# Optimization experiments

Hardware: AMD Instinct MI355X
Metric: run time of the kernel (lower is better)

The kernel has to match this reference:

```python
import jax, jax.numpy as jnp
import numpy as np

B, DIM1, DIM2, LATENT, T = 16, 1024, 1024, 512, 2048  # T == video_feat_dim
LN_EPS = 1e-5


def setup_inputs() -> dict:
    key = jax.random.key(0)
    ks = jax.random.split(key, 8)
    def xavier(k, shape):
        fan_out, fan_in = shape
        std = float(np.sqrt(2.0 / (fan_in + fan_out)))
        return jax.random.normal(k, shape, dtype=jnp.float32) * std
    return {
        "input1": jax.random.normal(ks[0], (B, DIM1, T), dtype=jnp.float32),
        "input2": jax.random.normal(ks[1], (B, DIM2, T), dtype=jnp.float32),
        "theta_w": xavier(ks[2], (LATENT, DIM2)),
        "theta_b": jnp.zeros((LATENT,), jnp.float32),
        "phi_w": xavier(ks[3], (LATENT, DIM1)),
        "phi_b": jnp.zeros((LATENT,), jnp.float32),
        "g_w": xavier(ks[4], (LATENT, DIM1)),
        "g_b": jnp.zeros((LATENT,), jnp.float32),
        "ln_gamma": jnp.ones((LATENT, T), jnp.float32),
        "ln_beta": jnp.zeros((LATENT, T), jnp.float32),
        "out_w": xavier(ks[5], (DIM2, LATENT)),
        "out_b": jnp.zeros((DIM2,), jnp.float32),
    }


def reference(input1, input2, theta_w, theta_b, phi_w, phi_b, g_w, g_b,
              ln_gamma, ln_beta, out_w, out_b):
    # 1x1 Conv1d == channel-wise matmul
    theta_x = jnp.einsum('ld,bdt->btl', theta_w, input2) + theta_b          # [B,T2,L]
    phi_x = jnp.einsum('ld,bdt->blt', phi_w, input1) + phi_b[:, None]       # [B,L,T1]
    scores = jnp.einsum('btl,bls->bts', theta_x, phi_x)                      # [B,T2,T1] (unscaled)
    p = jax.nn.softmax(scores, axis=-1)
    g_x = jnp.einsum('ld,bdt->btl', g_w, input1) + g_b                       # [B,T1,L]
    t_x = jnp.einsum('bts,bsl->blt', p, g_x)                                 # [B,L,T2]
    # LayerNorm over the last two dims jointly [LATENT, T]
    mu = jnp.mean(t_x, axis=(1, 2), keepdims=True)
    var = jnp.var(t_x, axis=(1, 2), keepdims=True)
    h = (t_x - mu) * jax.lax.rsqrt(var + LN_EPS) * ln_gamma + ln_beta
    h = jax.nn.relu(h)
    w_t = jnp.einsum('ol,blt->bot', out_w, h) + out_b[None, :, None]         # [B,DIM2,T2]
    return w_t + input2
```

## Files before the change

### kernel.cpp

```cpp
#include <hip/hip_runtime.h>
#include <hip/hip_bf16.h>

#define BB 16
#define D1 1024
#define D2 1024
#define LL 512
#define TT 2048
#define LN_EPS 1e-5f

typedef unsigned short u16;
typedef __attribute__((ext_vector_type(8))) _Float16 half8;
typedef __attribute__((ext_vector_type(4))) float f32x4;
typedef __attribute__((ext_vector_type(4))) unsigned int u32x4;

__device__ __forceinline__ u16 f2h(float v) {
    _Float16 h = (_Float16)v;
    return *(u16*)&h;
}
__device__ __forceinline__ float h2f(u16 u) {
    return (float)(*(const _Float16*)&u);
}

__device__ __forceinline__ void gload_lds16(const void* g, void* l) {
    __builtin_amdgcn_global_load_lds((const __attribute__((address_space(1))) void*)g,
                                     (__attribute__((address_space(3))) void*)l, 16, 0, 0);
}

#define MEMFENCE asm volatile("" ::: "memory")
__device__ __forceinline__ void block_barrier() {
    MEMFENCE; __builtin_amdgcn_s_barrier(); MEMFENCE;
}

template<int BIAS, int OMODE>
__global__ __launch_bounds__(512, 1) void nt_gemm(
    const u16* __restrict__ A, const u16* __restrict__ B,
    long sAb, long sBb, long sCb,
    int N, int Kd, int gx, int gy,
    const float* __restrict__ bias,
    void* __restrict__ out0,
    const float* __restrict__ resid, long sRb)
{
    __shared__ __align__(16) u16 smem[65536];

    const int nwg = gridDim.x;
    const int id = blockIdx.x;
    const int swz = (id & 7) * (nwg >> 3) + (id >> 3);
    const int bx = swz % gx;
    const int byz = swz / gx;
    const int by = byz % gy;
    const int b = byz / gy;

    const int tid = threadIdx.x;
    const long arow0 = (long)by * 256;
    const long brow0 = (long)bx * 256;
    const u16* Ab = A + (long)b * sAb + arow0 * Kd;
    const u16* Bb = B + (long)b * sBb + brow0 * Kd;

    const int wave = tid >> 6, lane = tid & 63;
    const int mh = wave >> 2;
    const int wm = mh * 128;
    const int wn = (wave & 3) * 64;
    const int lm = lane & 15, kg = lane >> 4;

    const int ntile = Kd >> 6;

    auto STAGE = [&](int buf, long k0) {
        u16* Ad = smem + buf * 32768;
        u16* Bd = Ad + 16384;
#pragma unroll
        for (int sw = 0; sw < 4; ++sw) {
            int idx = sw * 512 + tid;
            int m = idx >> 3, s = idx & 7;
            int gs = s ^ (m & 7);
            gload_lds16(Ab + k0 + (long)m * Kd + gs * 8, Ad + idx * 8);
        }
#pragma unroll
        for (int sw = 0; sw < 4; ++sw) {
            int idx = sw * 512 + tid;
            int m = idx >> 3, s = idx & 7;
            int gs = s ^ (m & 7);
            gload_lds16(Bb + k0 + (long)m * Kd + gs * 8, Bd + idx * 8);
        }
    };

    f32x4 acc[8][4];
#pragma unroll
    for (int i = 0; i < 8; ++i)
#pragma unroll
        for (int j = 0; j < 4; ++j) acc[i][j] = (f32x4){0.f, 0.f, 0.f, 0.f};

    STAGE(0, 0);
    if (ntile > 1) STAGE(1, 64);

    half8 a_[4][2], b_[2][2];

#define LOADA(ms_) do { \
    _Pragma("unroll") for (int f = 0; f < 4; ++f) \
    _Pragma("unroll") for (int kf = 0; kf < 2; ++kf) { \
        int mr = wm + (ms_) * 64 + f * 16 + lm; \
        int ss = (kf * 4 + kg) ^ (mr & 7); \
        a_[f][kf] = *(const half8*)(Ac + mr * 64 + ss * 8); } } while (0)
#define LOADB(ns_) do { \
    _Pragma("unroll") for (int f = 0; f < 2; ++f) \
    _Pragma("unroll") for (int kf = 0; kf < 2; ++kf) { \
        int nr = wn + (ns_) * 32 + f * 16 + lm; \
        int ss = (kf * 4 + kg) ^ (nr & 7); \
        b_[f][kf] = *(const half8*)(Bc + nr * 64 + ss * 8); } } while (0)
#define PH_MFMA(ms_, ns_) do { \
    block_barrier(); \
    asm volatile("s_waitcnt lgkmcnt(0)" ::: "memory"); \
    __builtin_amdgcn_sched_barrier(0); \
    __builtin_amdgcn_s_setprio(1); \
    _Pragma("unroll") for (int i = 0; i < 4; ++i) \
    _Pragma("unroll") for (int j = 0; j < 2; ++j) \
    _Pragma("unroll") for (int kf = 0; kf < 2; ++kf) \
        acc[(ms_) * 4 + i][(ns_) * 2 + j] = __builtin_amdgcn_mfma_f32_16x16x32_f16( \
            a_[i][kf], b_[j][kf], acc[(ms_) * 4 + i][(ns_) * 2 + j], 0, 0, 0); \
    __builtin_amdgcn_s_setprio(0); \
    block_barrier(); \
} while (0)

    for (int t = 0; t < ntile; ++t) {
        const int c = t & 1;
        const u16* Ac = smem + c * 32768;
        const u16* Bc = Ac + 16384;
        if (t + 1 < ntile) { asm volatile("s_waitcnt vmcnt(8)" ::: "memory"); }
        else               { asm volatile("s_waitcnt vmcnt(0)" ::: "memory"); }
        block_barrier();

        LOADA(0); LOADB(0); PH_MFMA(0, 0);
        LOADA(1);           PH_MFMA(1, 0);
        LOADB(1);           PH_MFMA(1, 1);
        LOADA(0);           PH_MFMA(0, 1);

        if (t + 2 < ntile) STAGE(c, (long)(t + 2) * 64);
    }
#undef LOADA
#undef LOADB
#undef PH_MFMA

    float* Cs = (float*)smem;
#pragma unroll
    for (int p = 0; p < 2; ++p) {
        __syncthreads();
        if (mh == p) {
#pragma unroll
            for (int ms = 0; ms < 2; ++ms)
#pragma unroll
                for (int i = 0; i < 4; ++i)
#pragma unroll
                    for (int ns = 0; ns < 2; ++ns)
#pragma unroll
                        for (int j = 0; j < 2; ++j)
#pragma unroll
                            for (int r = 0; r < 4; ++r) {
                                int row = ms * 64 + i * 16 + kg * 4 + r;
                                int col = wn + ns * 32 + j * 16 + lm;
                                Cs[row * 256 + (col ^ ((row & 7) << 2))] = acc[ms * 4 + i][ns * 2 + j][r];
                            }
        }
        __syncthreads();
        if (OMODE == 0 || OMODE == 3) {
#pragma unroll
            for (int it = 0; it < 16; ++it) {
                int elem = it * 512 + tid;
                int row = elem >> 6, c4 = elem & 63;
                int grow = (int)arow0 + p * 128 + row;
                int gcol = (int)brow0 + c4 * 4;
                f32x4 v = *(const f32x4*)&Cs[row * 256 + ((c4 ^ (row & 7)) << 2)];
                if (BIAS == 1) v += bias[grow];
                if (BIAS == 2) v += *(const f32x4*)(bias + gcol);
                long off = (long)b * sCb + (long)grow * N + gcol;
                if (OMODE == 3) {
                    f32x4 rv = __builtin_nontemporal_load(
                        (const f32x4*)(resid + (long)b * sRb + (long)grow * N + gcol));
                    v += rv;
                    __builtin_nontemporal_store(v, (f32x4*)((float*)out0 + off));
                } else {
                    *(f32x4*)((float*)out0 + off) = v;
                }
            }
        } else {
#pragma unroll
            for (int it = 0; it < 8; ++it) {
                int elem = it * 512 + tid;
                int row = elem >> 5, c8 = elem & 31;
                int grow = (int)arow0 + p * 128 + row;
                int gcol = (int)brow0 + c8 * 8;
                int g0 = (c8 * 2) ^ (row & 7);
                int g1 = (c8 * 2 + 1) ^ (row & 7);
                f32x4 u0 = *(const f32x4*)&Cs[row * 256 + g0 * 4];
                f32x4 u1 = *(const f32x4*)&Cs[row * 256 + g1 * 4];
                float vv[8] = {u0.x, u0.y, u0.z, u0.w, u1.x, u1.y, u1.z, u1.w};
                if (BIAS == 1) {
                    float bb = bias[grow];
#pragma unroll
                    for (int q = 0; q < 8; ++q) vv[q] += bb;
                }
                if (BIAS == 2) {
#pragma unroll
                    for (int q = 0; q < 8; ++q) vv[q] += bias[gcol + q];
                }
                union { u16 u[8]; u32x4 v4; } pk;
#pragma unroll
                for (int q = 0; q < 8; ++q) pk.u[q] = f2h(vv[q]);
                long off = (long)b * sCb + (long)grow * N + gcol;
                *(u32x4*)((u16*)out0 + off) = pk.v4;
            }
        }
    }
}

__global__ __launch_bounds__(256) void transpose_h(const float* __restrict__ in,
                                                   u16* __restrict__ o16, int D, int T) {
    __shared__ float tile[64][65];
    int b = blockIdx.z;
    const float* src = in + (long)b * D * T;
    long obase = (long)b * D * T;
    int t0 = blockIdx.x * 64, d0 = blockIdx.y * 64;
    int tx = threadIdx.x & 63, ty = threadIdx.x >> 6;
#pragma unroll
    for (int i = 0; i < 64; i += 4)
        tile[ty + i][tx] = __builtin_nontemporal_load(&src[(long)(d0 + ty + i) * T + t0 + tx]);
    __syncthreads();
#pragma unroll
    for (int i = 0; i < 64; i += 4) {
        long o = obase + (long)(t0 + ty + i) * D + d0 + tx;
        o16[o] = f2h(tile[tx][ty + i]);
    }
}

__global__ __launch_bounds__(256) void transpose_f32(const float* __restrict__ in,
                                                     float* __restrict__ out, int R, int C) {
    __shared__ float tile[64][65];
    int c0 = blockIdx.x * 64, r0 = blockIdx.y * 64;
    int tx = threadIdx.x & 63, ty = threadIdx.x >> 6;
#pragma unroll
    for (int i = 0; i < 64; i += 4)
        tile[ty + i][tx] = in[(long)(r0 + ty + i) * C + c0 + tx];
    __syncthreads();
#pragma unroll
    for (int i = 0; i < 64; i += 4)
        out[(long)(c0 + ty + i) * R + r0 + tx] = tile[tx][ty + i];
}

__global__ __launch_bounds__(256) void conv_w(const float* __restrict__ w,
                                              u16* __restrict__ h, int n) {
    int i = blockIdx.x * 256 + threadIdx.x;
    if (i < n) h[i] = f2h(w[i]);
}

__global__ __launch_bounds__(256) void softmax_rows(const float* __restrict__ S, u16* __restrict__ P) {
    long row = (long)blockIdx.z * TT + blockIdx.x;
    const float* s = S + row * TT;
    u16* p = P + row * TT;
    int tid = threadIdx.x;
    f32x4 v0 = *(const f32x4*)(s + tid * 8);
    f32x4 v1 = *(const f32x4*)(s + tid * 8 + 4);
    float x[8] = {v0.x, v0.y, v0.z, v0.w, v1.x, v1.y, v1.z, v1.w};
    float m = x[0];
#pragma unroll
    for (int j = 1; j < 8; ++j) m = fmaxf(m, x[j]);
#pragma unroll
    for (int off = 32; off; off >>= 1) m = fmaxf(m, __shfl_xor(m, off, 64));
    __shared__ float red[8];
    int wave = tid >> 6, lane = tid & 63;
    if (lane == 0) red[wave] = m;
    __syncthreads();
    m = fmaxf(fmaxf(red[0], red[1]), fmaxf(red[2], red[3]));
    float e[8]; float sum = 0.f;
#pragma unroll
    for (int j = 0; j < 8; ++j) { e[j] = __expf(x[j] - m); sum += e[j]; }
#pragma unroll
    for (int off = 32; off; off >>= 1) sum += __shfl_xor(sum, off, 64);
    if (lane == 0) red[4 + wave] = sum;
    __syncthreads();
    sum = red[4] + red[5] + red[6] + red[7];
    float inv = 1.f / sum;
    union { u16 u[8]; u32x4 v4; } pk;
#pragma unroll
    for (int j = 0; j < 8; ++j) pk.u[j] = f2h(e[j] * inv);
    *(u32x4*)(p + tid * 8) = pk.v4;
}

__global__ void zero32(float* p) { p[threadIdx.x] = 0.f; }

__global__ __launch_bounds__(256) void ln_partial(const u16* __restrict__ TXp, float* __restrict__ sums) {
    int b = blockIdx.z;
    const u16* x = TXp + (long)b * (LL * TT) + (long)blockIdx.x * 32768;
    int tid = threadIdx.x;
    float s = 0.f, sq = 0.f;
#pragma unroll 4
    for (int j = 0; j < 16; ++j) {
        u32x4 v = *(const u32x4*)(x + (j * 256 + tid) * 8);
        unsigned w[4] = {v.x, v.y, v.z, v.w};
#pragma unroll
        for (int q = 0; q < 4; ++q) {
            float a = h2f((u16)(w[q] & 0xffff));
            float c = h2f((u16)(w[q] >> 16));
            s += a + c;
            sq += a * a + c * c;
        }
    }
#pragma unroll
    for (int off = 32; off; off >>= 1) { s += __shfl_xor(s, off, 64); sq += __shfl_xor(sq, off, 64); }
    __shared__ float rs[8];
    int wave = tid >> 6, lane = tid & 63;
    if (lane == 0) { rs[wave] = s; rs[4 + wave] = sq; }
    __syncthreads();
    if (tid == 0) {
        atomicAdd(&sums[b * 2], rs[0] + rs[1] + rs[2] + rs[3]);
        atomicAdd(&sums[b * 2 + 1], rs[4] + rs[5] + rs[6] + rs[7]);
    }
}

__global__ __launch_bounds__(256) void ln_apply(const u16* __restrict__ TXp, const float* __restrict__ sums,
                                                const float* __restrict__ gT, const float* __restrict__ bT,
                                                u16* __restrict__ H) {
    int b = blockIdx.z;
    const float n = (float)(LL * TT);
    float mu = sums[b * 2] / n;
    float var = sums[b * 2 + 1] / n - mu * mu;
    float rstd = rsqrtf(var + LN_EPS);
    long base = (long)b * (LL * TT);
    long idx = ((long)blockIdx.x * 256 + threadIdx.x) * 8;
    u32x4 xv = *(const u32x4*)(TXp + base + idx);
    unsigned w[4] = {xv.x, xv.y, xv.z, xv.w};
    f32x4 g0 = *(const f32x4*)(gT + idx);
    f32x4 g1 = *(const f32x4*)(gT + idx + 4);
    f32x4 b0 = *(const f32x4*)(bT + idx);
    f32x4 b1 = *(const f32x4*)(bT + idx + 4);
    float g[8] = {g0.x, g0.y, g0.z, g0.w, g1.x, g1.y, g1.z, g1.w};
    float be[8] = {b0.x, b0.y, b0.z, b0.w, b1.x, b1.y, b1.z, b1.w};
    union { u16 u[8]; u32x4 v; } pk;
#pragma unroll
    for (int q = 0; q < 4; ++q) {
        float a = h2f((u16)(w[q] & 0xffff));
        float c = h2f((u16)(w[q] >> 16));
        float oa = fmaxf((a - mu) * rstd * g[q * 2] + be[q * 2], 0.f);
        float oc = fmaxf((c - mu) * rstd * g[q * 2 + 1] + be[q * 2 + 1], 0.f);
        pk.u[q * 2] = f2h(oa);
        pk.u[q * 2 + 1] = f2h(oc);
    }
    *(u32x4*)(H + base + idx) = pk.v;
}

extern "C" void kernel_launch(void* const* d_in, const int* in_sizes, int n_in,
                              void* d_out, int out_size, void* d_ws, size_t ws_size,
                              hipStream_t stream) {
    const float* input1  = (const float*)d_in[0];
    const float* input2  = (const float*)d_in[1];
    const float* theta_w = (const float*)d_in[2];
    const float* theta_b = (const float*)d_in[3];
    const float* phi_w   = (const float*)d_in[4];
    const float* phi_b   = (const float*)d_in[5];
    const float* g_w     = (const float*)d_in[6];
    const float* g_b     = (const float*)d_in[7];
    const float* ln_gamma= (const float*)d_in[8];
    const float* ln_beta = (const float*)d_in[9];
    const float* out_w   = (const float*)d_in[10];
    const float* out_b   = (const float*)d_in[11];
    float* out = (float*)d_out;

    char* ws = (char*)d_ws;
    const size_t MB = 1ull << 20;
    u16*  Xt     = (u16*)(ws + 0);
    float* scores= (float*)(ws + 0);
    u16*  pmat   = (u16*)(ws + 64 * MB);
    u16*  Qf     = (u16*)(ws + 192 * MB);
    u16*  Kf     = (u16*)(ws + 224 * MB);
    u16*  Vt     = (u16*)(ws + 256 * MB);
    u16*  TX     = (u16*)(ws + 288 * MB);
    u16*  H      = (u16*)(ws + 320 * MB);
    u16*  thw    = (u16*)(ws + 352 * MB);
    u16*  phw    = (u16*)(ws + 353 * MB);
    u16*  gww    = (u16*)(ws + 354 * MB);
    u16*  oww    = (u16*)(ws + 355 * MB);
    float* gammaT= (float*)(ws + 356 * MB);
    float* betaT = (float*)(ws + 360 * MB);
    float* sums  = (float*)(ws + 364 * MB);

    dim3 blk(256), blk5(512);

    conv_w<<<dim3((LL * D2 + 255) / 256), blk, 0, stream>>>(theta_w, thw, LL * D2);
    conv_w<<<dim3((LL * D1 + 255) / 256), blk, 0, stream>>>(phi_w, phw, LL * D1);
    conv_w<<<dim3((LL * D1 + 255) / 256), blk, 0, stream>>>(g_w, gww, LL * D1);
    conv_w<<<dim3((D2 * LL + 255) / 256), blk, 0, stream>>>(out_w, oww, D2 * LL);
    transpose_f32<<<dim3(TT / 64, LL / 64, 1), blk, 0, stream>>>(ln_gamma, gammaT, LL, TT);
    transpose_f32<<<dim3(TT / 64, LL / 64, 1), blk, 0, stream>>>(ln_beta, betaT, LL, TT);

    transpose_h<<<dim3(TT / 64, D2 / 64, BB), blk, 0, stream>>>(input2, Xt, D2, TT);
    nt_gemm<2, 1><<<dim3((LL / 256) * (TT / 256) * BB), blk5, 0, stream>>>(
        Xt, thw, (long)TT * D2, 0, (long)TT * LL, LL, D2, LL / 256, TT / 256,
        theta_b, Qf, nullptr, 0);

    transpose_h<<<dim3(TT / 64, D1 / 64, BB), blk, 0, stream>>>(input1, Xt, D1, TT);
    nt_gemm<2, 1><<<dim3((LL / 256) * (TT / 256) * BB), blk5, 0, stream>>>(
        Xt, phw, (long)TT * D1, 0, (long)TT * LL, LL, D1, LL / 256, TT / 256,
        phi_b, Kf, nullptr, 0);
    nt_gemm<1, 1><<<dim3((TT / 256) * (LL / 256) * BB), blk5, 0, stream>>>(
        gww, Xt, 0, (long)TT * D1, (long)LL * TT, TT, D1, TT / 256, LL / 256,
        g_b, Vt, nullptr, 0);

    for (int c = 0; c < 4; ++c) {
        long qoff = (long)c * 4 * TT * LL;
        nt_gemm<0, 0><<<dim3((TT / 256) * (TT / 256) * 4), blk5, 0, stream>>>(
            Qf + qoff, Kf + qoff, (long)TT * LL, (long)TT * LL, (long)TT * TT,
            TT, LL, TT / 256, TT / 256, nullptr, scores, nullptr, 0);
        softmax_rows<<<dim3(TT, 1, 4), blk, 0, stream>>>(scores, pmat + (long)c * 4 * TT * TT);
    }
    nt_gemm<0, 1><<<dim3((LL / 256) * (TT / 256) * BB), blk5, 0, stream>>>(
        pmat, Vt, (long)TT * TT, (long)LL * TT, (long)TT * LL,
        LL, TT, LL / 256, TT / 256, nullptr, TX, nullptr, 0);

    zero32<<<dim3(1), dim3(32), 0, stream>>>(sums);
    ln_partial<<<dim3(32, 1, BB), blk, 0, stream>>>(TX, sums);
    ln_apply<<<dim3(512, 1, BB), blk, 0, stream>>>(TX, sums, gammaT, betaT, H);

    nt_gemm<1, 3><<<dim3((TT / 256) * (D2 / 256) * BB), blk5, 0, stream>>>(
        oww, H, 0, (long)TT * LL, (long)D2 * TT, TT, LL, TT / 256, D2 / 256,
        out_b, out, input2, (long)D2 * TT);
}
```

Measured before the change: 603.3 us.

## Add 128x128 GEMM variant and interleave P·V per chunk to shrink probability buffer

```diff
diff --git a/kernel.cpp b/kernel.cpp
--- a/kernel.cpp
+++ b/kernel.cpp
@@ -211,6 +211,146 @@
     }
 }
 
+__device__ __forceinline__ void stage_tile_sm(const u16* __restrict__ g, int ldk, u16* lds, int tid) {
+#pragma unroll
+    for (int it = 0; it < 4; ++it) {
+        int idx = it * 256 + tid;
+        int m = idx >> 3, s = idx & 7;
+        int gs = s ^ (m & 7);
+        gload_lds16(g + (long)m * ldk + gs * 8, lds + idx * 8);
+    }
+}
+
+template<int BIAS, int OMODE>
+__global__ __launch_bounds__(256, 4) void nt_gemm_sm(
+    const u16* __restrict__ A, const u16* __restrict__ B,
+    long sAb, long sBb, long sCb,
+    int N, int Kd, int gx, int gy,
+    const float* __restrict__ bias,
+    void* __restrict__ out0,
+    const float* __restrict__ resid, long sRb)
+{
+    __shared__ __align__(16) u16 smem[2 * 128 * 64];
+    u16* As = smem;
+    u16* Bs = smem + 128 * 64;
+
+    const int nwg = gridDim.x;
+    const int id = blockIdx.x;
+    const int swz = (id & 7) * (nwg >> 3) + (id >> 3);
+    const int bx = swz % gx;
+    const int byz = swz / gx;
+    const int by = byz % gy;
+    const int b = byz / gy;
+
+    const int tid = threadIdx.x;
+    const long arow0 = (long)by * 128;
+    const long brow0 = (long)bx * 128;
+    const u16* Ab = A + (long)b * sAb + arow0 * Kd;
+    const u16* Bb = B + (long)b * sBb + brow0 * Kd;
+
+    const int wave = tid >> 6, lane = tid & 63;
+    const int wm = (wave >> 1) * 64, wn = (wave & 1) * 64;
+    const int lm = lane & 15, kg = lane >> 4;
+
+    f32x4 acc[4][4];
+#pragma unroll
+    for (int i = 0; i < 4; ++i)
+#pragma unroll
+        for (int j = 0; j < 4; ++j) acc[i][j] = (f32x4){0.f, 0.f, 0.f, 0.f};
+
+    for (int k0 = 0; k0 < Kd; k0 += 64) {
+        stage_tile_sm(Ab + k0, Kd, As, tid);
+        stage_tile_sm(Bb + k0, Kd, Bs, tid);
+        __syncthreads();
+#pragma unroll
+        for (int ks = 0; ks < 2; ++ks) {
+            half8 af[4], bf[4];
+#pragma unroll
+            for (int f = 0; f < 4; ++f) {
+                int mr = wm + f * 16 + lm;
+                int as_ = (ks * 4 + kg) ^ (mr & 7);
+                af[f] = *(const half8*)(As + mr * 64 + as_ * 8);
+                int nr = wn + f * 16 + lm;
+                int bs_ = (ks * 4 + kg) ^ (nr & 7);
+                bf[f] = *(const half8*)(Bs + nr * 64 + bs_ * 8);
+            }
+#pragma unroll
+            for (int i = 0; i < 4; ++i)
+#pragma unroll
+                for (int j = 0; j < 4; ++j)
+                    acc[i][j] = __builtin_amdgcn_mfma_f32_16x16x32_f16(af[i], bf[j], acc[i][j], 0, 0, 0);
+        }
+        __syncthreads();
+    }
+
+    float* Cs = (float*)smem;
+#pragma unroll
+    for (int p = 0; p < 2; ++p) {
+        if (p) __syncthreads();
+        if (wm == p * 64) {
+#pragma unroll
+            for (int i = 0; i < 4; ++i)
+#pragma unroll
+                for (int j = 0; j < 4; ++j)
+#pragma unroll
+                    for (int r = 0; r < 4; ++r) {
+                        int row = i * 16 + kg * 4 + r;
+                        int col = wn + j * 16 + lm;
+                        Cs[row * 128 + (col ^ ((row & 7) << 2))] = acc[i][j][r];
+                    }
+        }
+        __syncthreads();
+        if (OMODE == 0 || OMODE == 3) {
+#pragma unroll
+            for (int rr = 0; rr < 8; ++rr) {
+                int elem = rr * 256 + tid;
+                int row = elem >> 5, c4 = elem & 31;
+                int grow = (int)arow0 + p * 64 + row;
+                int gcol = (int)brow0 + c4 * 4;
+                f32x4 v = *(const f32x4*)&Cs[row * 128 + ((c4 ^ (row & 7)) << 2)];
+                if (BIAS == 1) v += bias[grow];
+                if (BIAS == 2) v += *(const f32x4*)(bias + gcol);
+                long off = (long)b * sCb + (long)grow * N + gcol;
+                if (OMODE == 3) {
+                    f32x4 rv = __builtin_nontemporal_load(
+                        (const f32x4*)(resid + (long)b * sRb + (long)grow * N + gcol));
+                    v += rv;
+                    __builtin_nontemporal_store(v, (f32x4*)((float*)out0 + off));
+                } else {
+                    *(f32x4*)((float*)out0 + off) = v;
+                }
+            }
+        } else {
+#pragma unroll
+            for (int rr = 0; rr < 4; ++rr) {
+                int elem = rr * 256 + tid;
+                int row = elem >> 4, c8 = elem & 15;
+                int grow = (int)arow0 + p * 64 + row;
+                int gcol = (int)brow0 + c8 * 8;
+                int g0 = (c8 * 2) ^ (row & 7);
+                int g1 = (c8 * 2 + 1) ^ (row & 7);
+                f32x4 u0 = *(const f32x4*)&Cs[row * 128 + g0 * 4];
+                f32x4 u1 = *(const f32x4*)&Cs[row * 128 + g1 * 4];
+                float vv[8] = {u0.x, u0.y, u0.z, u0.w, u1.x, u1.y, u1.z, u1.w};
+                if (BIAS == 1) {
+                    float bb = bias[grow];
+#pragma unroll
+                    for (int q = 0; q < 8; ++q) vv[q] += bb;
+                }
+                if (BIAS == 2) {
+#pragma unroll
+                    for (int q = 0; q < 8; ++q) vv[q] += bias[gcol + q];
+                }
+                union { u16 u[8]; u32x4 v4; } pk;
+#pragma unroll
+                for (int q = 0; q < 8; ++q) pk.u[q] = f2h(vv[q]);
+                long off = (long)b * sCb + (long)grow * N + gcol;
+                *(u32x4*)((u16*)out0 + off) = pk.v4;
+            }
+        }
+    }
+}
+
 __global__ __launch_bounds__(256) void transpose_h(const float* __restrict__ in,
                                                    u16* __restrict__ o16, int D, int T) {
     __shared__ float tile[64][65];
@@ -367,18 +507,18 @@
     u16*  Xt     = (u16*)(ws + 0);
     float* scores= (float*)(ws + 0);
     u16*  pmat   = (u16*)(ws + 64 * MB);
-    u16*  Qf     = (u16*)(ws + 192 * MB);
-    u16*  Kf     = (u16*)(ws + 224 * MB);
-    u16*  Vt     = (u16*)(ws + 256 * MB);
-    u16*  TX     = (u16*)(ws + 288 * MB);
-    u16*  H      = (u16*)(ws + 320 * MB);
-    u16*  thw    = (u16*)(ws + 352 * MB);
-    u16*  phw    = (u16*)(ws + 353 * MB);
-    u16*  gww    = (u16*)(ws + 354 * MB);
-    u16*  oww    = (u16*)(ws + 355 * MB);
-    float* gammaT= (float*)(ws + 356 * MB);
-    float* betaT = (float*)(ws + 360 * MB);
-    float* sums  = (float*)(ws + 364 * MB);
+    u16*  Qf     = (u16*)(ws + 96 * MB);
+    u16*  Kf     = (u16*)(ws + 128 * MB);
+    u16*  Vt     = (u16*)(ws + 160 * MB);
+    u16*  TX     = (u16*)(ws + 192 * MB);
+    u16*  H      = (u16*)(ws + 224 * MB);
+    u16*  thw    = (u16*)(ws + 256 * MB);
+    u16*  phw    = (u16*)(ws + 257 * MB);
+    u16*  gww    = (u16*)(ws + 258 * MB);
+    u16*  oww    = (u16*)(ws + 259 * MB);
+    float* gammaT= (float*)(ws + 260 * MB);
+    float* betaT = (float*)(ws + 264 * MB);
+    float* sums  = (float*)(ws + 268 * MB);
 
     dim3 blk(256), blk5(512);
 
@@ -390,16 +530,16 @@
     transpose_f32<<<dim3(TT / 64, LL / 64, 1), blk, 0, stream>>>(ln_beta, betaT, LL, TT);
 
     transpose_h<<<dim3(TT / 64, D2 / 64, BB), blk, 0, stream>>>(input2, Xt, D2, TT);
-    nt_gemm<2, 1><<<dim3((LL / 256) * (TT / 256) * BB), blk5, 0, stream>>>(
-        Xt, thw, (long)TT * D2, 0, (long)TT * LL, LL, D2, LL / 256, TT / 256,
+    nt_gemm_sm<2, 1><<<dim3((LL / 128) * (TT / 128) * BB), blk, 0, stream>>>(
+        Xt, thw, (long)TT * D2, 0, (long)TT * LL, LL, D2, LL / 128, TT / 128,
         theta_b, Qf, nullptr, 0);
 
     transpose_h<<<dim3(TT / 64, D1 / 64, BB), blk, 0, stream>>>(input1, Xt, D1, TT);
-    nt_gemm<2, 1><<<dim3((LL / 256) * (TT / 256) * BB), blk5, 0, stream>>>(
-        Xt, phw, (long)TT * D1, 0, (long)TT * LL, LL, D1, LL / 256, TT / 256,
+    nt_gemm_sm<2, 1><<<dim3((LL / 128) * (TT / 128) * BB), blk, 0, stream>>>(
+        Xt, phw, (long)TT * D1, 0, (long)TT * LL, LL, D1, LL / 128, TT / 128,
         phi_b, Kf, nullptr, 0);
-    nt_gemm<1, 1><<<dim3((TT / 256) * (LL / 256) * BB), blk5, 0, stream>>>(
-        gww, Xt, 0, (long)TT * D1, (long)LL * TT, TT, D1, TT / 256, LL / 256,
+    nt_gemm_sm<1, 1><<<dim3((TT / 128) * (LL / 128) * BB), blk, 0, stream>>>(
+        gww, Xt, 0, (long)TT * D1, (long)LL * TT, TT, D1, TT / 128, LL / 128,
         g_b, Vt, nullptr, 0);
 
     for (int c = 0; c < 4; ++c) {
@@ -407,17 +547,17 @@
         nt_gemm<0, 0><<<dim3((TT / 256) * (TT / 256) * 4), blk5, 0, stream>>>(
             Qf + qoff, Kf + qoff, (long)TT * LL, (long)TT * LL, (long)TT * TT,
             TT, LL, TT / 256, TT / 256, nullptr, scores, nullptr, 0);
-        softmax_rows<<<dim3(TT, 1, 4), blk, 0, stream>>>(scores, pmat + (long)c * 4 * TT * TT);
-    }
-    nt_gemm<0, 1><<<dim3((LL / 256) * (TT / 256) * BB), blk5, 0, stream>>>(
-        pmat, Vt, (long)TT * TT, (long)LL * TT, (long)TT * LL,
-        LL, TT, LL / 256, TT / 256, nullptr, TX, nullptr, 0);
+        softmax_rows<<<dim3(TT, 1, 4), blk, 0, stream>>>(scores, pmat);
+        nt_gemm_sm<0, 1><<<dim3((LL / 128) * (TT / 128) * 4), blk, 0, stream>>>(
+            pmat, Vt + (long)c * 4 * LL * TT, (long)TT * TT, (long)LL * TT, (long)TT * LL,
+            LL, TT, LL / 128, TT / 128, nullptr, TX + qoff, nullptr, 0);
+    }
 
     zero32<<<dim3(1), dim3(32), 0, stream>>>(sums);
     ln_partial<<<dim3(32, 1, BB), blk, 0, stream>>>(TX, sums);
     ln_apply<<<dim3(512, 1, BB), blk, 0, stream>>>(TX, sums, gammaT, betaT, H);
 
-    nt_gemm<1, 3><<<dim3((TT / 256) * (D2 / 256) * BB), blk5, 0, stream>>>(
-        oww, H, 0, (long)TT * LL, (long)D2 * TT, TT, LL, TT / 256, D2 / 256,
+    nt_gemm_sm<1, 3><<<dim3((TT / 128) * (D2 / 128) * BB), blk, 0, stream>>>(
+        oww, H, 0, (long)TT * LL, (long)D2 * TT, TT, LL, TT / 128, D2 / 128,
         out_b, out, input2, (long)D2 * TT);
 }
```

After: 638.4 us. +5.8%, slower.
